# Performance work log

Hardware: AMD Instinct MI355X
Metric: run time of the kernel (lower is better)

## Reference

```python
import jax, jax.numpy as jnp
import numpy as np

BN_EPS = 1e-5

def _gin_conv(x, src, dst, w1, b1, g, bt, mu, var, w2, b2):
    # GINConv, eps=0: h = MLP(x + sum_{j in N(i)} x_j)
    n = x.shape[0]
    agg = jax.ops.segment_sum(x[src], dst, num_segments=n)  # [N, d]
    h = x + agg
    h = h @ w1 + b1
    # BatchNorm1d (eval mode, running stats)
    h = (h - mu) * jax.lax.rsqrt(var + BN_EPS) * g + bt
    h = jax.nn.elu(h)
    h = h @ w2 + b2
    return jax.nn.elu(h)

def setup_inputs() -> dict:
    key = jax.random.key(0)
    N, E, D_IN, H, OUT = 40000, 600000, 128, 128, 64
    ks = jax.random.split(key, 40)
    ki = iter(range(40))
    inp = {}
    inp['x'] = jax.random.normal(ks[next(ki)], (N, D_IN), dtype=jnp.float32)
    inp['edge_index'] = jax.random.randint(ks[next(ki)], (2, E), 0, N, dtype=jnp.int64)
    def lin(k, fin, fout):
        k1, k2 = jax.random.split(k)
        w = jax.random.normal(k1, (fin, fout), dtype=jnp.float32) / np.sqrt(fin)
        b = jax.random.normal(k2, (fout,), dtype=jnp.float32) * 0.01
        return w, b
    for i, fin in zip((1, 2, 3), (D_IN, H, H)):
        w1, b1 = lin(ks[next(ki)], fin, H)
        w2, b2 = lin(ks[next(ki)], H, H)
        g = 1.0 + 0.1 * jax.random.normal(ks[next(ki)], (H,), dtype=jnp.float32)
        bt = 0.1 * jax.random.normal(ks[next(ki)], (H,), dtype=jnp.float32)
        mu = 0.1 * jax.random.normal(ks[next(ki)], (H,), dtype=jnp.float32)
        var = jax.random.uniform(ks[next(ki)], (H,), dtype=jnp.float32, minval=0.5, maxval=1.5)
        inp.update({f'c{i}_w1': w1, f'c{i}_b1': b1, f'c{i}_g': g, f'c{i}_bt': bt,
                    f'c{i}_mu': mu, f'c{i}_var': var, f'c{i}_w2': w2, f'c{i}_b2': b2})
    inp['lin1_w'], inp['lin1_b'] = lin(ks[next(ki)], H, H)
    inp['lin2_w'], inp['lin2_b'] = lin(ks[next(ki)], H, OUT)
    return inp

def reference(x, edge_index,
              c1_w1, c1_b1, c1_g, c1_bt, c1_mu, c1_var, c1_w2, c1_b2,
              c2_w1, c2_b1, c2_g, c2_bt, c2_mu, c2_var, c2_w2, c2_b2,
              c3_w1, c3_b1, c3_g, c3_bt, c3_mu, c3_var, c3_w2, c3_b2,
              lin1_w, lin1_b, lin2_w, lin2_b):
    src, dst = edge_index[0], edge_index[1]
    h = _gin_conv(x, src, dst, c1_w1, c1_b1, c1_g, c1_bt, c1_mu, c1_var, c1_w2, c1_b2)
    h = _gin_conv(h, src, dst, c2_w1, c2_b1, c2_g, c2_bt, c2_mu, c2_var, c2_w2, c2_b2)
    h = _gin_conv(h, src, dst, c3_w1, c3_b1, c3_g, c3_bt, c3_mu, c3_var, c3_w2, c3_b2)
    h = jax.nn.elu(h @ lin1_w + lin1_b)
    # dropout p=0.5 is identity in eval mode
    return h @ lin2_w + lin2_b
```

## Files before the change

kernel.cpp:

```cpp
#include <hip/hip_runtime.h>
#include <cmath>

#define NODES 40000
#define NPAD  40960
#define EDGES 600000
#define HD    128
#define CAP   80
#define BN_EPS 1e-5f
#define PK    (HD + 8)

typedef short bf16x8 __attribute__((ext_vector_type(8)));
typedef float f32x4  __attribute__((ext_vector_type(4)));
typedef unsigned short u16;
typedef unsigned int   u32;

__device__ __forceinline__ float bf2f(u16 u) {
  union { u32 i; float f; } v; v.i = ((u32)u) << 16; return v.f;
}
__device__ __forceinline__ u16 f2bf(float f) {
  union { float f; u32 i; } v; v.f = f;
  u32 r = v.i + 0x7FFF + ((v.i >> 16) & 1);
  return (u16)(r >> 16);
}
__device__ __forceinline__ float elu(float x) {
  return x > 0.f ? x : __expf(x) - 1.f;
}

struct WPrep { const float* s[8]; u16* d[8]; };

__global__ __launch_bounds__(256) void prep_all(const float4* __restrict__ x4,
                                                ushort4* __restrict__ xb4,
                                                WPrep p, int* __restrict__ cnt) {
  const int bid = blockIdx.x;
  const int tid = threadIdx.x;
  if (bid < 5000) {
    int i = bid * 256 + tid;
    float4 v = x4[i];
    ushort4 o;
    o.x = f2bf(v.x); o.y = f2bf(v.y); o.z = f2bf(v.z); o.w = f2bf(v.w);
    xb4[i] = o;
  } else if (bid < 5128) {
    int b = bid - 5000;
    int m = b >> 4, xx = b & 15;
    int N = (m == 7) ? 64 : 128;
    int tiles_n = N / 32;
    int tx = xx % tiles_n, tk = xx / tiles_n;
    if (tk >= 4) return;
    __shared__ float t[32][33];
    int c = tid & 31, r8 = tid >> 5;
    const float* s = p.s[m];
    for (int rr = 0; rr < 32; rr += 8)
      t[rr + r8][c] = s[(size_t)(tk * 32 + rr + r8) * N + tx * 32 + c];
    __syncthreads();
    u16* d = p.d[m];
    for (int rr = 0; rr < 32; rr += 8)
      d[(size_t)(tx * 32 + rr + r8) * HD + tk * 32 + c] = f2bf(t[c][rr + r8]);
  } else {
    int i = (bid - 5128) * 256 + tid;
    if (i < NODES) cnt[i] = 0;
  }
}

__global__ __launch_bounds__(256) void bucket_fill(const int* __restrict__ ei,
                                                   int* __restrict__ cnt,
                                                   int* __restrict__ bucket) {
  int e = blockIdx.x * 256 + threadIdx.x;
  if (e >= EDGES) return;
  int s = ei[e];
  int d = ei[EDGES + e];
  int pos = atomicAdd(&cnt[d], 1);
  if (pos < CAP) bucket[d * CAP + pos] = s;
}

__device__ __forceinline__ void unpack_init(float* a, uint4 v) {
  a[0] = bf2f((u16)v.x); a[1] = bf2f((u16)(v.x >> 16));
  a[2] = bf2f((u16)v.y); a[3] = bf2f((u16)(v.y >> 16));
  a[4] = bf2f((u16)v.z); a[5] = bf2f((u16)(v.z >> 16));
  a[6] = bf2f((u16)v.w); a[7] = bf2f((u16)(v.w >> 16));
}
__device__ __forceinline__ void unpack_add(float* a, uint4 v) {
  a[0] += bf2f((u16)v.x); a[1] += bf2f((u16)(v.x >> 16));
  a[2] += bf2f((u16)v.y); a[3] += bf2f((u16)(v.y >> 16));
  a[4] += bf2f((u16)v.z); a[5] += bf2f((u16)(v.z >> 16));
  a[6] += bf2f((u16)v.w); a[7] += bf2f((u16)(v.w >> 16));
}

__device__ __forceinline__ void gather64(const u16* __restrict__ x,
                                         const int* __restrict__ cnt,
                                         const int* __restrict__ bucket,
                                         int node0, int tid,
                                         u16 (*L)[PK]) {
  const int ql = tid & 15;
  const int qw = tid >> 4;
  for (int r = 0; r < 4; ++r) {
    const int brow = qw * 4 + r;
    const int node = node0 + brow;
    float a[8];
    if (node < NODES) {
      const int i0 = node * CAP;
      uint4 self = ((const uint4*)(x + (size_t)node * HD))[ql];
      int sv = bucket[i0 + ql];
      int deg = cnt[node];
      if (deg > CAP) deg = CAP;
      unpack_init(a, self);
      for (int c0 = 0; c0 < deg; c0 += 16) {
        int m = deg - c0;
        if (m > 16) m = 16;
        for (int j = 0; j < m; j += 8) {
          int idx[8];
          uint4 uu[8];
#pragma unroll
          for (int jj = 0; jj < 8; ++jj) {
            int src = j + jj < m ? j + jj : 0;
            idx[jj] = __shfl(sv, src, 16);
          }
#pragma unroll
          for (int jj = 0; jj < 8; ++jj)
            uu[jj] = ((const uint4*)(x + (size_t)idx[jj] * HD))[ql];
#pragma unroll
          for (int jj = 0; jj < 8; ++jj)
            if (j + jj < m) unpack_add(a, uu[jj]);
        }
        int nc = c0 + 16;
        if (nc < deg) {
          int ad = nc + ql;
          sv = bucket[i0 + (ad < CAP ? ad : 0)];
        }
      }
    } else {
#pragma unroll
      for (int k = 0; k < 8; ++k) a[k] = 0.f;
    }
    uint4 pk;
    pk.x = (u32)f2bf(a[0]) | ((u32)f2bf(a[1]) << 16);
    pk.y = (u32)f2bf(a[2]) | ((u32)f2bf(a[3]) << 16);
    pk.z = (u32)f2bf(a[4]) | ((u32)f2bf(a[5]) << 16);
    pk.w = (u32)f2bf(a[6]) | ((u32)f2bf(a[7]) << 16);
    *(uint4*)&L[128 + brow][ql * 8] = pk;
  }
}

__global__ __launch_bounds__(256) void gin_layer(
    const u16* __restrict__ xin, const int* __restrict__ cnt,
    const int* __restrict__ bucket, const u16* __restrict__ W1t,
    const float* __restrict__ b1, const float* __restrict__ g,
    const float* __restrict__ bt, const float* __restrict__ mu,
    const float* __restrict__ vr, const u16* __restrict__ W2t,
    const float* __restrict__ b2, u16* __restrict__ xout) {
  __shared__ u16 L[192][PK];

  const int tid = threadIdx.x;
  const int wv = tid >> 6, lane = tid & 63;
  const int col = lane & 15, kg = lane >> 4;
  const int strip = blockIdx.x * 4 + wv;
  const int hrow = 128 + wv * 16;

#pragma unroll
  for (int t = tid; t < 128 * 16; t += 256) {
    int r = t >> 4, c8 = t & 15;
    *(bf16x8*)&L[r][c8 * 8] = *(const bf16x8*)(W1t + (size_t)r * HD + c8 * 8);
  }
  gather64(xin, cnt, bucket, blockIdx.x * 64, tid, L);
  __syncthreads();

  f32x4 acc[8];
#pragma unroll
  for (int t = 0; t < 8; ++t) acc[t] = (f32x4){0.f, 0.f, 0.f, 0.f};
#pragma unroll
  for (int kk = 0; kk < HD; kk += 32) {
    bf16x8 av = *(const bf16x8*)&L[hrow + col][kk + kg * 8];
#pragma unroll
    for (int t = 0; t < 8; ++t) {
      bf16x8 bv = *(const bf16x8*)&L[t * 16 + col][kk + kg * 8];
      acc[t] = __builtin_amdgcn_mfma_f32_16x16x32_bf16(av, bv, acc[t], 0, 0, 0);
    }
  }
  __syncthreads();

#pragma unroll
  for (int t = tid; t < 128 * 16; t += 256) {
    int r = t >> 4, c8 = t & 15;
    *(bf16x8*)&L[r][c8 * 8] = *(const bf16x8*)(W2t + (size_t)r * HD + c8 * 8);
  }
#pragma unroll
  for (int t = 0; t < 8; ++t) {
    int c = t * 16 + col;
    float rs = rsqrtf(vr[c] + BN_EPS) * g[c];
    float bb = bt[c] + (b1[c] - mu[c]) * rs;
#pragma unroll
    for (int r = 0; r < 4; ++r)
      L[hrow + kg * 4 + r][c] = f2bf(elu(acc[t][r] * rs + bb));
  }
  __syncthreads();

  f32x4 acc2[8];
#pragma unroll
  for (int t = 0; t < 8; ++t) acc2[t] = (f32x4){0.f, 0.f, 0.f, 0.f};
#pragma unroll
  for (int kk = 0; kk < HD; kk += 32) {
    bf16x8 av = *(const bf16x8*)&L[hrow + col][kk + kg * 8];
#pragma unroll
    for (int t = 0; t < 8; ++t) {
      bf16x8 bv = *(const bf16x8*)&L[t * 16 + col][kk + kg * 8];
      acc2[t] = __builtin_amdgcn_mfma_f32_16x16x32_bf16(av, bv, acc2[t], 0, 0, 0);
    }
  }
#pragma unroll
  for (int t = 0; t < 8; ++t) {
    int c = t * 16 + col;
    float bb = b2[c];
#pragma unroll
    for (int r = 0; r < 4; ++r)
      L[hrow + kg * 4 + r][c] = f2bf(elu(acc2[t][r] + bb));
  }
  {
    int r0 = lane >> 4, seg = lane & 15;
#pragma unroll
    for (int rr = 0; rr < 16; rr += 4) {
      int row = rr + r0;
      *(float4*)((char*)(xout + (size_t)(strip * 16 + row) * HD) + seg * 16) =
          *(const float4*)((const char*)&L[hrow + row][0] + seg * 16);
    }
  }
}

__global__ __launch_bounds__(256) void gin_head(
    const u16* __restrict__ xin, const int* __restrict__ cnt,
    const int* __restrict__ bucket, const u16* __restrict__ W1t,
    const float* __restrict__ b1, const float* __restrict__ g,
    const float* __restrict__ bt, const float* __restrict__ mu,
    const float* __restrict__ vr, const u16* __restrict__ W2t,
    const float* __restrict__ b2, const u16* __restrict__ L1t,
    const float* __restrict__ lb1, const u16* __restrict__ L2t,
    const float* __restrict__ lb2, float* __restrict__ out) {
  __shared__ u16 L[192][PK];

  const int tid = threadIdx.x;
  const int wv = tid >> 6, lane = tid & 63;
  const int col = lane & 15, kg = lane >> 4;
  const int strip = blockIdx.x * 4 + wv;
  const int hrow = 128 + wv * 16;

#pragma unroll
  for (int t = tid; t < 128 * 16; t += 256) {
    int r = t >> 4, c8 = t & 15;
    *(bf16x8*)&L[r][c8 * 8] = *(const bf16x8*)(W1t + (size_t)r * HD + c8 * 8);
  }
  gather64(xin, cnt, bucket, blockIdx.x * 64, tid, L);
  __syncthreads();

  f32x4 acc[8];
#pragma unroll
  for (int t = 0; t < 8; ++t) acc[t] = (f32x4){0.f, 0.f, 0.f, 0.f};
#pragma unroll
  for (int kk = 0; kk < HD; kk += 32) {
    bf16x8 av = *(const bf16x8*)&L[hrow + col][kk + kg * 8];
#pragma unroll
    for (int t = 0; t < 8; ++t) {
      bf16x8 bv = *(const bf16x8*)&L[t * 16 + col][kk + kg * 8];
      acc[t] = __builtin_amdgcn_mfma_f32_16x16x32_bf16(av, bv, acc[t], 0, 0, 0);
    }
  }
  __syncthreads();
#pragma unroll
  for (int t = tid; t < 128 * 16; t += 256) {
    int r = t >> 4, c8 = t & 15;
    *(bf16x8*)&L[r][c8 * 8] = *(const bf16x8*)(W2t + (size_t)r * HD + c8 * 8);
  }
#pragma unroll
  for (int t = 0; t < 8; ++t) {
    int c = t * 16 + col;
    float rs = rsqrtf(vr[c] + BN_EPS) * g[c];
    float bb = bt[c] + (b1[c] - mu[c]) * rs;
#pragma unroll
    for (int r = 0; r < 4; ++r)
      L[hrow + kg * 4 + r][c] = f2bf(elu(acc[t][r] * rs + bb));
  }
  __syncthreads();

#pragma unroll
  for (int t = 0; t < 8; ++t) acc[t] = (f32x4){0.f, 0.f, 0.f, 0.f};
#pragma unroll
  for (int kk = 0; kk < HD; kk += 32) {
    bf16x8 av = *(const bf16x8*)&L[hrow + col][kk + kg * 8];
#pragma unroll
    for (int t = 0; t < 8; ++t) {
      bf16x8 bv = *(const bf16x8*)&L[t * 16 + col][kk + kg * 8];
      acc[t] = __builtin_amdgcn_mfma_f32_16x16x32_bf16(av, bv, acc[t], 0, 0, 0);
    }
  }
  __syncthreads();
#pragma unroll
  for (int t = tid; t < 128 * 16; t += 256) {
    int r = t >> 4, c8 = t & 15;
    *(bf16x8*)&L[r][c8 * 8] = *(const bf16x8*)(L1t + (size_t)r * HD + c8 * 8);
  }
#pragma unroll
  for (int t = 0; t < 8; ++t) {
    int c = t * 16 + col;
    float bb = b2[c];
#pragma unroll
    for (int r = 0; r < 4; ++r)
      L[hrow + kg * 4 + r][c] = f2bf(elu(acc[t][r] + bb));
  }
  __syncthreads();

#pragma unroll
  for (int t = 0; t < 8; ++t) acc[t] = (f32x4){0.f, 0.f, 0.f, 0.f};
#pragma unroll
  for (int kk = 0; kk < HD; kk += 32) {
    bf16x8 av = *(const bf16x8*)&L[hrow + col][kk + kg * 8];
#pragma unroll
    for (int t = 0; t < 8; ++t) {
      bf16x8 bv = *(const bf16x8*)&L[t * 16 + col][kk + kg * 8];
      acc[t] = __builtin_amdgcn_mfma_f32_16x16x32_bf16(av, bv, acc[t], 0, 0, 0);
    }
  }
  __syncthreads();
#pragma unroll
  for (int t = tid; t < 64 * 16; t += 256) {
    int r = t >> 4, c8 = t & 15;
    *(bf16x8*)&L[r][c8 * 8] = *(const bf16x8*)(L2t + (size_t)r * HD + c8 * 8);
  }
#pragma unroll
  for (int t = 0; t < 8; ++t) {
    int c = t * 16 + col;
    float bb = lb1[c];
#pragma unroll
    for (int r = 0; r < 4; ++r)
      L[hrow + kg * 4 + r][c] = f2bf(elu(acc[t][r] + bb));
  }
  __syncthreads();

  f32x4 acc2[4];
#pragma unroll
  for (int t = 0; t < 4; ++t) acc2[t] = (f32x4){0.f, 0.f, 0.f, 0.f};
#pragma unroll
  for (int kk = 0; kk < HD; kk += 32) {
    bf16x8 av = *(const bf16x8*)&L[hrow + col][kk + kg * 8];
#pragma unroll
    for (int t = 0; t < 4; ++t) {
      bf16x8 bv = *(const bf16x8*)&L[t * 16 + col][kk + kg * 8];
      acc2[t] = __builtin_amdgcn_mfma_f32_16x16x32_bf16(av, bv, acc2[t], 0, 0, 0);
    }
  }
#pragma unroll
  for (int t = 0; t < 4; ++t) {
    int c = t * 16 + col;
    float bb = lb2[c];
#pragma unroll
    for (int r = 0; r < 4; ++r)
      ((float*)&L[hrow + kg * 4 + r][0])[c] = acc2[t][r] + bb;
  }
  if (strip < NODES / 16) {
    int r0 = lane >> 4, seg = lane & 15;
#pragma unroll
    for (int rr = 0; rr < 16; rr += 4) {
      int row = rr + r0;
      *(float4*)((char*)(out + (size_t)(strip * 16 + row) * 64) + seg * 16) =
          *(const float4*)((const char*)&L[hrow + row][0] + seg * 16);
    }
  }
}

extern "C" void kernel_launch(void* const* d_in, const int* in_sizes, int n_in,
                              void* d_out, int out_size, void* d_ws, size_t ws_size,
                              hipStream_t stream) {
  const float* x = (const float*)d_in[0];
  const int* ei  = (const int*)d_in[1];
  const float* p[30];
  for (int i = 0; i < 30 && i < n_in; ++i) p[i] = (const float*)d_in[i];

  const size_t FEATP = (size_t)NPAD * HD;
  u16* xb0  = (u16*)d_ws;
  u16* xb1  = xb0 + FEATP;
  u16* wt   = xb1 + FEATP;
  u16* wts[8];
  for (int m = 0; m < 8; ++m) wts[m] = wt + (size_t)m * HD * HD;
  int* cnt    = (int*)(wt + 8 * HD * HD);
  int* bucket = cnt + NODES;

  dim3 blk(256);
  const int edgeGrid = (EDGES + 255) / 256;
  const int layerGrid = NPAD / 64;

  WPrep wp;
  const int widx[8] = {2, 8, 10, 16, 18, 24, 26, 28};
  for (int m = 0; m < 8; ++m) { wp.s[m] = p[widx[m]]; wp.d[m] = wts[m]; }
  prep_all<<<5285, blk, 0, stream>>>((const float4*)x, (ushort4*)xb0, wp, cnt);
  bucket_fill<<<edgeGrid, blk, 0, stream>>>(ei, cnt, bucket);

  gin_layer<<<layerGrid, blk, 0, stream>>>(
      xb0, cnt, bucket, wts[0], p[3], p[4], p[5], p[6], p[7], wts[1], p[9], xb1);
  gin_layer<<<layerGrid, blk, 0, stream>>>(
      xb1, cnt, bucket, wts[2], p[11], p[12], p[13], p[14], p[15], wts[3], p[17], xb0);
  gin_head<<<layerGrid, blk, 0, stream>>>(
      xb0, cnt, bucket, wts[4], p[19], p[20], p[21], p[22], p[23], wts[5], p[25],
      wts[6], p[27], wts[7], p[29], (float*)d_out);
}
```

Before: 257.8 us.

## Load-balance neighbor gather with LDS work queue and shrink bucket to 16-bit

The 16-lane groups in each block no longer process a fixed 4 rows of the 64-node tile. Each group now claims the next node from a shared-memory atomic counter, so groups that hit high-degree nodes do not stall the rest of the block at the barrier. The neighbor bucket array is also stored as 16-bit indices, which is valid because node ids are below 65536. This halves bucket traffic and footprint. The cost is one LDS atomic plus a shuffle per node and an extra barrier to initialise the counter.

```diff
diff --git a/kernel.cpp b/kernel.cpp
--- a/kernel.cpp
+++ b/kernel.cpp
@@ -63,13 +63,13 @@
 
 __global__ __launch_bounds__(256) void bucket_fill(const int* __restrict__ ei,
                                                    int* __restrict__ cnt,
-                                                   int* __restrict__ bucket) {
+                                                   u16* __restrict__ bucket) {
   int e = blockIdx.x * 256 + threadIdx.x;
   if (e >= EDGES) return;
   int s = ei[e];
   int d = ei[EDGES + e];
   int pos = atomicAdd(&cnt[d], 1);
-  if (pos < CAP) bucket[d * CAP + pos] = s;
+  if (pos < CAP) bucket[d * CAP + pos] = (u16)s;
 }
 
 __device__ __forceinline__ void unpack_init(float* a, uint4 v) {
@@ -87,14 +87,17 @@
 
 __device__ __forceinline__ void gather64(const u16* __restrict__ x,
                                          const int* __restrict__ cnt,
-                                         const int* __restrict__ bucket,
+                                         const u16* __restrict__ bucket,
                                          int node0, int tid,
-                                         u16 (*L)[PK]) {
+                                         u16 (*L)[PK], int* __restrict__ wq) {
   const int ql = tid & 15;
-  const int qw = tid >> 4;
-  for (int r = 0; r < 4; ++r) {
-    const int brow = qw * 4 + r;
-    const int node = node0 + brow;
+  const int qwl = (tid >> 4) & 3;
+  for (;;) {
+    int n = 0;
+    if (ql == 0) n = atomicAdd(wq, 1);
+    n = __shfl(n, qwl * 16, 64);
+    if (n >= 64) break;
+    const int node = node0 + n;
     float a[8];
     if (node < NODES) {
       const int i0 = node * CAP;
@@ -136,18 +139,19 @@
     pk.y = (u32)f2bf(a[2]) | ((u32)f2bf(a[3]) << 16);
     pk.z = (u32)f2bf(a[4]) | ((u32)f2bf(a[5]) << 16);
     pk.w = (u32)f2bf(a[6]) | ((u32)f2bf(a[7]) << 16);
-    *(uint4*)&L[128 + brow][ql * 8] = pk;
+    *(uint4*)&L[128 + n][ql * 8] = pk;
   }
 }
 
 __global__ __launch_bounds__(256) void gin_layer(
     const u16* __restrict__ xin, const int* __restrict__ cnt,
-    const int* __restrict__ bucket, const u16* __restrict__ W1t,
+    const u16* __restrict__ bucket, const u16* __restrict__ W1t,
     const float* __restrict__ b1, const float* __restrict__ g,
     const float* __restrict__ bt, const float* __restrict__ mu,
     const float* __restrict__ vr, const u16* __restrict__ W2t,
     const float* __restrict__ b2, u16* __restrict__ xout) {
   __shared__ u16 L[192][PK];
+  __shared__ int wq;
 
   const int tid = threadIdx.x;
   const int wv = tid >> 6, lane = tid & 63;
@@ -155,12 +159,15 @@
   const int strip = blockIdx.x * 4 + wv;
   const int hrow = 128 + wv * 16;
 
+  if (tid == 0) wq = 0;
+  __syncthreads();
+
 #pragma unroll
   for (int t = tid; t < 128 * 16; t += 256) {
     int r = t >> 4, c8 = t & 15;
     *(bf16x8*)&L[r][c8 * 8] = *(const bf16x8*)(W1t + (size_t)r * HD + c8 * 8);
   }
-  gather64(xin, cnt, bucket, blockIdx.x * 64, tid, L);
+  gather64(xin, cnt, bucket, blockIdx.x * 64, tid, L, &wq);
   __syncthreads();
 
   f32x4 acc[8];
@@ -226,7 +233,7 @@
 
 __global__ __launch_bounds__(256) void gin_head(
     const u16* __restrict__ xin, const int* __restrict__ cnt,
-    const int* __restrict__ bucket, const u16* __restrict__ W1t,
+    const u16* __restrict__ bucket, const u16* __restrict__ W1t,
     const float* __restrict__ b1, const float* __restrict__ g,
     const float* __restrict__ bt, const float* __restrict__ mu,
     const float* __restrict__ vr, const u16* __restrict__ W2t,
@@ -234,6 +241,7 @@
     const float* __restrict__ lb1, const u16* __restrict__ L2t,
     const float* __restrict__ lb2, float* __restrict__ out) {
   __shared__ u16 L[192][PK];
+  __shared__ int wq;
 
   const int tid = threadIdx.x;
   const int wv = tid >> 6, lane = tid & 63;
@@ -241,12 +249,15 @@
   const int strip = blockIdx.x * 4 + wv;
   const int hrow = 128 + wv * 16;
 
+  if (tid == 0) wq = 0;
+  __syncthreads();
+
 #pragma unroll
   for (int t = tid; t < 128 * 16; t += 256) {
     int r = t >> 4, c8 = t & 15;
     *(bf16x8*)&L[r][c8 * 8] = *(const bf16x8*)(W1t + (size_t)r * HD + c8 * 8);
   }
-  gather64(xin, cnt, bucket, blockIdx.x * 64, tid, L);
+  gather64(xin, cnt, bucket, blockIdx.x * 64, tid, L, &wq);
   __syncthreads();
 
   f32x4 acc[8];
@@ -377,8 +388,8 @@
   u16* wt   = xb1 + FEATP;
   u16* wts[8];
   for (int m = 0; m < 8; ++m) wts[m] = wt + (size_t)m * HD * HD;
-  int* cnt    = (int*)(wt + 8 * HD * HD);
-  int* bucket = cnt + NODES;
+  int* cnt     = (int*)(wt + 8 * HD * HD);
+  u16* bucket  = (u16*)(cnt + NODES);
 
   dim3 blk(256);
   const int edgeGrid = (EDGES + 255) / 256;
```

Result: no change. 259.2 us (+0.6%).
